# Optimization experiments

Measured on AMD Instinct MI355X. Metric: run time of the kernel, lower is better.

Reference implementation:

```python
import jax, jax.numpy as jnp
import numpy as np

X_SCALE, X_ZP = 0.03, -66.0
Y_SCALE, Y_ZP = 0.025, 160.0  # per-tensor quant params for uint8 y


def setup_inputs() -> dict:
    key = jax.random.key(0)
    kx, ky = jax.random.split(key)
    # x simulates int8 values in [-128, 127], stored as fp32
    x = jax.random.randint(kx, (7, 8, 1024, 1024), 0, 256).astype(jnp.float32) - 128.0
    # y simulates uint8 values in [0, 255], stored as fp32
    y = jax.random.randint(ky, (8, 1024, 1024), 0, 256).astype(jnp.float32)
    return {"x": x, "y": y}


def reference(x, y):
    # dequantize: (q - zero_point) * scale
    qx = (x - X_ZP) * X_SCALE              # [7, B, M, K] fp32
    qy = (y - Y_ZP) * Y_SCALE              # [B, K, N] fp32
    # torch.matmul broadcasting: 4D @ 3D -> [7, B, M, N]
    return jnp.einsum('sbmk,bkn->sbmn', qx, qy)
```

## Files before the change

kernel.cpp:

```cpp
#include <hip/hip_runtime.h>
#include <cstdint>


#define NG 56

typedef int v4i  __attribute__((ext_vector_type(4)));
typedef int v16i __attribute__((ext_vector_type(16)));

#define GLOAD16(g, l) __builtin_amdgcn_global_load_lds( \
    (const __attribute__((address_space(1))) void*)(g), \
    (__attribute__((address_space(3))) void*)(l), 16, 0, 0)

#define MFMA_I8(a, b, c) __builtin_amdgcn_mfma_i32_32x32x32_i8(a, b, c, 0, 0, 0)

typedef __attribute__((address_space(3))) const unsigned char* lds_cptr;

__device__ __forceinline__ v4i lds_read16(lds_cptr p) {
    v4i d;
    asm volatile("ds_read_b128 %0, %1" : "=v"(d) : "v"(p));
    return d;
}

__device__ __forceinline__ unsigned pack4(float4 v, float& s) {
    s += (v.x + v.y) + (v.z + v.w);
    unsigned b0 = __float_as_uint(v.x + 8388736.0f);
    unsigned b1 = __float_as_uint(v.y + 8388736.0f);
    unsigned b2 = __float_as_uint(v.z + 8388736.0f);
    unsigned b3 = __float_as_uint(v.w + 8388736.0f);
    return ((b0 & 0xFFu) | ((b1 & 0xFFu) << 8) | ((b2 & 0xFFu) << 16) | ((b3 & 0xFFu) << 24))
           ^ 0x80808080u;
}

__global__ __launch_bounds__(256) void k_prep_x(const float* __restrict__ x,
                                                unsigned char* __restrict__ xb,
                                                float* __restrict__ rx) {
    int row  = blockIdx.x * 4 + (threadIdx.x >> 6);
    int lane = threadIdx.x & 63;
    const float* src = x + (size_t)row * 1024;
    float s = 0.f;
#pragma unroll
    for (int it = 0; it < 4; ++it) {
        float4 v = *(const float4*)(src + it * 256 + lane * 4);
        unsigned p = pack4(v, s);
        *(unsigned*)&xb[(size_t)row * 1024 + it * 256 + lane * 4] = p;
    }
#pragma unroll
    for (int off = 32; off > 0; off >>= 1) s += __shfl_down(s, off);
    if (lane == 0) rx[row] = s;
}

__global__ __launch_bounds__(256) void k_prep_y(const float* __restrict__ y,
                                                unsigned char* __restrict__ yt,
                                                float* __restrict__ cy) {
    __shared__ float tile[64][65];
    __shared__ float csum[4][64];
    int b  = blockIdx.x >> 8;
    int t  = blockIdx.x & 255;
    int kt = (t >> 4) * 64, nt = (t & 15) * 64;
    int tx = threadIdx.x & 63;
    int ty = threadIdx.x >> 6;
    const float* src = y + ((size_t)b << 20) + (size_t)kt * 1024 + nt;
    float part = 0.f;
#pragma unroll
    for (int r = 0; r < 16; ++r) {
        int kk = r * 4 + ty;
        float v = src[(size_t)kk * 1024 + tx];
        tile[kk][tx] = v;
        part += v;
    }
    csum[ty][tx] = part;
    __syncthreads();
    if (threadIdx.x < 64) {
        float s = csum[0][tx] + csum[1][tx] + csum[2][tx] + csum[3][tx];
        atomicAdd(&cy[b * 1024 + nt + tx], s);
    }
    int ky = threadIdx.x & 15;
    int ny = threadIdx.x >> 4;
#pragma unroll
    for (int r = 0; r < 4; ++r) {
        int nn = r * 16 + ny;
        unsigned b0 = __float_as_uint(tile[ky * 4 + 0][nn] + 8388608.0f);
        unsigned b1 = __float_as_uint(tile[ky * 4 + 1][nn] + 8388608.0f);
        unsigned b2 = __float_as_uint(tile[ky * 4 + 2][nn] + 8388608.0f);
        unsigned b3 = __float_as_uint(tile[ky * 4 + 3][nn] + 8388608.0f);
        unsigned p = ((b0 & 0xFFu) | ((b1 & 0xFFu) << 8) | ((b2 & 0xFFu) << 16) |
                      ((b3 & 0xFFu) << 24)) ^ 0x80808080u;
        *(unsigned*)&yt[((size_t)b << 20) + (size_t)(nt + nn) * 1024 + kt + ky * 4] = p;
    }
}

__global__ __launch_bounds__(512, 2) void k_gemm(const unsigned char* __restrict__ xb,
                                                 const unsigned char* __restrict__ yt,
                                                 const float* __restrict__ rx,
                                                 const float* __restrict__ cy,
                                                 float* __restrict__ out) {
    __shared__ __align__(16) unsigned char As[3][256 * 64];
    __shared__ __align__(16) unsigned char Bs[3][256 * 64];

    int bid = blockIdx.x;
    int wg  = (bid & 7) * 112 + (bid >> 3);
    int g   = wg >> 4;
    int t   = wg & 15;
    int m0  = (t >> 2) * 256, n0 = (t & 3) * 256;
    int b   = g & 7;

    int tid = threadIdx.x, lane = tid & 63, w = tid >> 6;
    int wm = w >> 2, wn = w & 3;

    const unsigned char* Ab = xb + (size_t)g * 1048576 + (size_t)m0 * 1024;
    const unsigned char* Bb = yt + ((size_t)b << 20) + (size_t)n0 * 1024;

    int srow   = tid >> 2;
    int schunk = (tid & 3) ^ ((srow >> 1) & 3);
    size_t offA0 = (size_t)srow * 1024 + (size_t)schunk * 16;
    size_t offA1 = offA0 + 131072;
    int dstA0 = (tid & ~63) * 16;
    int dstA1 = 8192 + (tid & ~63) * 16;

#define GLQ0(rs, kb) GLOAD16(Ab + offA0 + (size_t)(kb), &As[rs][dstA0])
#define GLQ1(rs, kb) GLOAD16(Ab + offA1 + (size_t)(kb), &As[rs][dstA1])
#define GLQ2(rs, kb) GLOAD16(Bb + offA0 + (size_t)(kb), &Bs[rs][dstA0])
#define GLQ3(rs, kb) GLOAD16(Bb + offA1 + (size_t)(kb), &Bs[rs][dstA1])

    v16i acc[4][2];
#pragma unroll
    for (int i = 0; i < 4; ++i)
#pragma unroll
        for (int j = 0; j < 2; ++j)
#pragma unroll
            for (int q = 0; q < 16; ++q) acc[i][j][q] = 0;

    int arow = lane & 31, hi = lane >> 5, key = (lane >> 1) & 3;
    int rA0 = (wm * 128 +  0 + arow) * 64;
    int rA1 = (wm * 128 + 32 + arow) * 64;
    int rA2 = (wm * 128 + 64 + arow) * 64;
    int rA3 = (wm * 128 + 96 + arow) * 64;
    int rB0 = (wn * 64 +  0 + arow) * 64;
    int rB1 = (wn * 64 + 32 + arow) * 64;
    int c0 = (hi ^ key) * 16;
    int c1 = ((2 + hi) ^ key) * 16;

    v4i cA0, cA1, cB0, cB1;
    v4i nA0, nA1, nB0, nB1;

#define VM3 asm volatile("s_waitcnt vmcnt(3)" ::: "memory")
#define VM0 asm volatile("s_waitcnt vmcnt(0)" ::: "memory")
#define NOVM (void)0

#define PHASE(VMS, RN, CK, RAa, RAb, N0, N1, N2, N3, GLS, LGK, HH, C0_, C1_, C2_, C3_) do { \
    VMS;                                                                   \
    __builtin_amdgcn_s_barrier();                                          \
    __builtin_amdgcn_sched_barrier(0);                                     \
    { lds_cptr _ap = (lds_cptr)&As[RN][0];                                 \
      lds_cptr _bp = (lds_cptr)&Bs[RN][0];                                 \
      N0 = lds_read16(_ap + RAa + (CK));                                   \
      N1 = lds_read16(_ap + RAb + (CK));                                   \
      N2 = lds_read16(_bp + rB0 + (CK));                                   \
      N3 = lds_read16(_bp + rB1 + (CK)); }                                 \
    GLS;                                                                   \
    asm volatile("s_waitcnt lgkmcnt(" #LGK ")" ::: "memory");              \
    __builtin_amdgcn_sched_barrier(0);                                     \
    __builtin_amdgcn_s_setprio(1);                                         \
    acc[2*(HH)  ][0] = MFMA_I8(C0_, C2_, acc[2*(HH)  ][0]);                \
    acc[2*(HH)  ][1] = MFMA_I8(C0_, C3_, acc[2*(HH)  ][1]);                \
    acc[2*(HH)+1][0] = MFMA_I8(C1_, C2_, acc[2*(HH)+1][0]);                \
    acc[2*(HH)+1][1] = MFMA_I8(C1_, C3_, acc[2*(HH)+1][1]);                \
    __builtin_amdgcn_s_setprio(0);                                         \
} while (0)

#define TILE(rt, rn, rs, DOST, VMP3) do {                                                       \
    PHASE(NOVM, rt, c0, rA2, rA3, nA0,nA1,nB0,nB1, if (DOST) GLQ0(rs, kb);, 4, 0, cA0,cA1,cB0,cB1); \
    PHASE(NOVM, rt, c1, rA0, rA1, cA0,cA1,cB0,cB1, if (DOST) GLQ1(rs, kb);, 4, 1, nA0,nA1,nB0,nB1); \
    PHASE(NOVM, rt, c1, rA2, rA3, nA0,nA1,nB0,nB1, if (DOST) GLQ2(rs, kb);, 4, 0, cA0,cA1,cB0,cB1); \
    PHASE(VMP3, rn, c0, rA0, rA1, cA0,cA1,cB0,cB1, if (DOST) GLQ3(rs, kb);, 4, 1, nA0,nA1,nB0,nB1); \
} while (0)

    GLQ0(0, 0);  GLQ1(0, 0);  GLQ2(0, 0);  GLQ3(0, 0);
    GLQ0(1, 64); GLQ1(1, 64); GLQ2(1, 64); GLQ3(1, 64);
    VM3; VM0;
    asm volatile("s_waitcnt vmcnt(4)" ::: "memory");
    __builtin_amdgcn_s_barrier();
    __builtin_amdgcn_sched_barrier(0);
    { lds_cptr _ap = (lds_cptr)&As[0][0];
      lds_cptr _bp = (lds_cptr)&Bs[0][0];
      cA0 = lds_read16(_ap + rA0 + c0);
      cA1 = lds_read16(_ap + rA1 + c0);
      cB0 = lds_read16(_bp + rB0 + c0);
      cB1 = lds_read16(_bp + rB1 + c0); }

    int kb = 128;
    for (int u = 0; u < 4; ++u) {
        TILE(0, 1, 2, 1, VM3); kb += 64;
        TILE(1, 2, 0, 1, VM3); kb += 64;
        TILE(2, 0, 1, 1, VM3); kb += 64;
    }
    TILE(0, 1, 2, 1, VM3); kb += 64;
    TILE(1, 2, 0, 1, VM3); kb += 64;
    TILE(2, 0, 1, 0, VM0);
    PHASE(NOVM, 0, c0, rA2, rA3, nA0,nA1,nB0,nB1, NOVM;, 4, 0, cA0,cA1,cB0,cB1);
    PHASE(NOVM, 0, c1, rA0, rA1, cA0,cA1,cB0,cB1, NOVM;, 4, 1, nA0,nA1,nB0,nB1);
    PHASE(NOVM, 0, c1, rA2, rA3, nA0,nA1,nB0,nB1, NOVM;, 4, 0, cA0,cA1,cB0,cB1);
    __builtin_amdgcn_s_barrier();
    __builtin_amdgcn_sched_barrier(0);
    asm volatile("s_waitcnt lgkmcnt(0)" ::: "memory");
    __builtin_amdgcn_sched_barrier(0);
    acc[2][0] = MFMA_I8(nA0, nB0, acc[2][0]);
    acc[2][1] = MFMA_I8(nA0, nB1, acc[2][1]);
    acc[3][0] = MFMA_I8(nA1, nB0, acc[3][0]);
    acc[3][1] = MFMA_I8(nA1, nB1, acc[3][1]);
#undef TILE
#undef PHASE
#undef VM3
#undef VM0
#undef NOVM
#undef GLQ0
#undef GLQ1
#undef GLQ2
#undef GLQ3

    const float* rxp = rx + g * 1024 + m0 + wm * 128;
    const float* cyp = cy + b * 1024 + n0 + wn * 64;
    float* og = out + (size_t)g * 1048576 + (size_t)(m0 + wm * 128) * 1024 + n0 + wn * 64;
    int col = lane & 31, r4 = hi * 4;
#pragma unroll
    for (int fi = 0; fi < 4; ++fi)
#pragma unroll
        for (int fj = 0; fj < 2; ++fj) {
            int cc = fj * 32 + col;
            float cv = cyp[cc];
            v16i v = acc[fi][fj];
#pragma unroll
            for (int q = 0; q < 16; ++q) {
                int rl = (q & 3) + 8 * (q >> 2) + r4;
                float rxv = rxp[fi * 32 + rl];
                og[(size_t)(fi * 32 + rl) * 1024 + cc] =
                    7.5e-4f * ((float)v[q] - 32.0f * rxv + 66.0f * cv - 10813440.0f);
            }
        }
}

__global__ void k_naive(const float* __restrict__ x, const float* __restrict__ y,
                        float* __restrict__ out) {
    int g = blockIdx.z, b = g & 7;
    int tx = threadIdx.x, ty = threadIdx.y;
    int m = blockIdx.y * 16 + ty, n = blockIdx.x * 16 + tx;
    __shared__ float a[16][17], bs[16][17];
    float s = 0.f;
    for (int kt = 0; kt < 64; ++kt) {
        a[ty][tx]  = x[(size_t)g * 1048576 + (size_t)m * 1024 + kt * 16 + tx];
        bs[ty][tx] = y[(size_t)b * 1048576 + (size_t)(kt * 16 + ty) * 1024 + n];
        __syncthreads();
#pragma unroll
        for (int j = 0; j < 16; ++j)
            s += ((a[ty][j] + 66.0f) * 0.03f) * ((bs[j][tx] - 160.0f) * 0.025f);
        __syncthreads();
    }
    out[(size_t)g * 1048576 + (size_t)m * 1024 + n] = s;
}

extern "C" void kernel_launch(void* const* d_in, const int* in_sizes, int n_in,
                              void* d_out, int out_size, void* d_ws, size_t ws_size,
                              hipStream_t stream) {
    const float* x = (const float*)d_in[0];
    const float* y = (const float*)d_in[1];
    float* out = (float*)d_out;

    const size_t CY_OFF = 0;
    const size_t RX_OFF = 32768;
    const size_t YT_OFF = 262144;
    const size_t XB_OFF = 262144 + 8388608ull;
    const size_t NEED   = XB_OFF + 58720256ull;

    if (ws_size >= NEED) {
        float* cy         = (float*)((char*)d_ws + CY_OFF);
        float* rx         = (float*)((char*)d_ws + RX_OFF);
        unsigned char* yt = (unsigned char*)((char*)d_ws + YT_OFF);
        unsigned char* xb = (unsigned char*)((char*)d_ws + XB_OFF);
        hipMemsetAsync(cy, 0, 32768, stream);
        k_prep_x<<<14336, 256, 0, stream>>>(x, xb, rx);
        k_prep_y<<<2048, 256, 0, stream>>>(y, yt, cy);
        k_gemm<<<NG * 16, 512, 0, stream>>>(xb, yt, rx, cy, out);
    } else {
        dim3 grid(64, 64, NG), blk(16, 16);
        k_naive<<<grid, blk, 0, stream>>>(x, y, out);
    }
}
```

Before: 181.9 us.

## Load B fragments directly from global into registers and quad-buffer A in LDS

B is no longer staged through LDS. Each wave now loads its B fragments straight into registers with global_load_dwordx4, double-buffered across K steps, while only A goes through LDS with four stages instead of three. The inner loop is restructured so each step reads all A fragments, issues the next B loads and the A prefetch, then runs 16 MFMAs. This removes the B LDS writes and reads and halves LDS use. In exchange the two waves that share a column of B both fetch it from cache, register pressure rises, and global load latency now sits directly in front of the MFMAs.

Measured after the change: 214.6 us. 1.18x slower.

```diff
diff --git a/kernel.cpp b/kernel.cpp
--- a/kernel.cpp
+++ b/kernel.cpp
@@ -94,8 +94,7 @@
                                                  const float* __restrict__ rx,
                                                  const float* __restrict__ cy,
                                                  float* __restrict__ out) {
-    __shared__ __align__(16) unsigned char As[3][256 * 64];
-    __shared__ __align__(16) unsigned char Bs[3][256 * 64];
+    __shared__ __align__(16) unsigned char As[4][256 * 64];
 
     int bid = blockIdx.x;
     int wg  = (bid & 7) * 112 + (bid >> 3);
@@ -108,7 +107,6 @@
     int wm = w >> 2, wn = w & 3;
 
     const unsigned char* Ab = xb + (size_t)g * 1048576 + (size_t)m0 * 1024;
-    const unsigned char* Bb = yt + ((size_t)b << 20) + (size_t)n0 * 1024;
 
     int srow   = tid >> 2;
     int schunk = (tid & 3) ^ ((srow >> 1) & 3);
@@ -117,10 +115,10 @@
     int dstA0 = (tid & ~63) * 16;
     int dstA1 = 8192 + (tid & ~63) * 16;
 
-#define GLQ0(rs, kb) GLOAD16(Ab + offA0 + (size_t)(kb), &As[rs][dstA0])
-#define GLQ1(rs, kb) GLOAD16(Ab + offA1 + (size_t)(kb), &As[rs][dstA1])
-#define GLQ2(rs, kb) GLOAD16(Bb + offA0 + (size_t)(kb), &Bs[rs][dstA0])
-#define GLQ3(rs, kb) GLOAD16(Bb + offA1 + (size_t)(kb), &Bs[rs][dstA1])
+#define STAGE(buf, kbyte) do {                                    \
+    GLOAD16(Ab + offA0 + (size_t)(kbyte), &As[buf][dstA0]);       \
+    GLOAD16(Ab + offA1 + (size_t)(kbyte), &As[buf][dstA1]);       \
+} while (0)
 
     v16i acc[4][2];
 #pragma unroll
@@ -135,88 +133,80 @@
     int rA1 = (wm * 128 + 32 + arow) * 64;
     int rA2 = (wm * 128 + 64 + arow) * 64;
     int rA3 = (wm * 128 + 96 + arow) * 64;
-    int rB0 = (wn * 64 +  0 + arow) * 64;
-    int rB1 = (wn * 64 + 32 + arow) * 64;
     int c0 = (hi ^ key) * 16;
     int c1 = ((2 + hi) ^ key) * 16;
 
-    v4i cA0, cA1, cB0, cB1;
-    v4i nA0, nA1, nB0, nB1;
-
-#define VM3 asm volatile("s_waitcnt vmcnt(3)" ::: "memory")
-#define VM0 asm volatile("s_waitcnt vmcnt(0)" ::: "memory")
-#define NOVM (void)0
-
-#define PHASE(VMS, RN, CK, RAa, RAb, N0, N1, N2, N3, GLS, LGK, HH, C0_, C1_, C2_, C3_) do { \
-    VMS;                                                                   \
-    __builtin_amdgcn_s_barrier();                                          \
-    __builtin_amdgcn_sched_barrier(0);                                     \
-    { lds_cptr _ap = (lds_cptr)&As[RN][0];                                 \
-      lds_cptr _bp = (lds_cptr)&Bs[RN][0];                                 \
-      N0 = lds_read16(_ap + RAa + (CK));                                   \
-      N1 = lds_read16(_ap + RAb + (CK));                                   \
-      N2 = lds_read16(_bp + rB0 + (CK));                                   \
-      N3 = lds_read16(_bp + rB1 + (CK)); }                                 \
-    GLS;                                                                   \
-    asm volatile("s_waitcnt lgkmcnt(" #LGK ")" ::: "memory");              \
-    __builtin_amdgcn_sched_barrier(0);                                     \
-    __builtin_amdgcn_s_setprio(1);                                         \
-    acc[2*(HH)  ][0] = MFMA_I8(C0_, C2_, acc[2*(HH)  ][0]);                \
-    acc[2*(HH)  ][1] = MFMA_I8(C0_, C3_, acc[2*(HH)  ][1]);                \
-    acc[2*(HH)+1][0] = MFMA_I8(C1_, C2_, acc[2*(HH)+1][0]);                \
-    acc[2*(HH)+1][1] = MFMA_I8(C1_, C3_, acc[2*(HH)+1][1]);                \
-    __builtin_amdgcn_s_setprio(0);                                         \
+    const unsigned char* Bbl = yt + ((size_t)b << 20)
+                             + (size_t)(n0 + wn * 64 + arow) * 1024 + hi * 16;
+
+#define LOADB(R0, R1, R2, R3, kbyte) do {                                             \
+    const unsigned char* _bp = Bbl + (size_t)(kbyte);                                 \
+    asm volatile("global_load_dwordx4 %0, %1, off" : "=&v"(R0) : "v"(_bp) : "memory");          \
+    asm volatile("global_load_dwordx4 %0, %1, off" : "=&v"(R1) : "v"(_bp + 32) : "memory");     \
+    asm volatile("global_load_dwordx4 %0, %1, off" : "=&v"(R2) : "v"(_bp + 32768) : "memory");  \
+    asm volatile("global_load_dwordx4 %0, %1, off" : "=&v"(R3) : "v"(_bp + 32800) : "memory");  \
 } while (0)
 
-#define TILE(rt, rn, rs, DOST, VMP3) do {                                                       \
-    PHASE(NOVM, rt, c0, rA2, rA3, nA0,nA1,nB0,nB1, if (DOST) GLQ0(rs, kb);, 4, 0, cA0,cA1,cB0,cB1); \
-    PHASE(NOVM, rt, c1, rA0, rA1, cA0,cA1,cB0,cB1, if (DOST) GLQ1(rs, kb);, 4, 1, nA0,nA1,nB0,nB1); \
-    PHASE(NOVM, rt, c1, rA2, rA3, nA0,nA1,nB0,nB1, if (DOST) GLQ2(rs, kb);, 4, 0, cA0,cA1,cB0,cB1); \
-    PHASE(VMP3, rn, c0, rA0, rA1, cA0,cA1,cB0,cB1, if (DOST) GLQ3(rs, kb);, 4, 1, nA0,nA1,nB0,nB1); \
+#define STEP(T, VMN, BU0, BU1, BU2, BU3, BL0, BL1, BL2, BL3, DOLB, DOST) do { \
+    asm volatile("s_waitcnt vmcnt(" #VMN ")" ::: "memory");                   \
+    __builtin_amdgcn_s_barrier();                                             \
+    __builtin_amdgcn_sched_barrier(0);                                        \
+    lds_cptr _ap = (lds_cptr)&As[(T) & 3][0];                                 \
+    v4i a00 = lds_read16(_ap + rA0 + c0);                                     \
+    v4i a10 = lds_read16(_ap + rA1 + c0);                                     \
+    v4i a20 = lds_read16(_ap + rA2 + c0);                                     \
+    v4i a30 = lds_read16(_ap + rA3 + c0);                                     \
+    v4i a01 = lds_read16(_ap + rA0 + c1);                                     \
+    v4i a11 = lds_read16(_ap + rA1 + c1);                                     \
+    v4i a21 = lds_read16(_ap + rA2 + c1);                                     \
+    v4i a31 = lds_read16(_ap + rA3 + c1);                                     \
+    if (DOLB) { LOADB(BL0, BL1, BL2, BL3, ((T) + 1) * 64); }                  \
+    __builtin_amdgcn_sched_barrier(0);                                        \
+    if (DOST) { STAGE(((T) + 3) & 3, ((T) + 3) * 64); }                       \
+    __builtin_amdgcn_sched_barrier(0);                                        \
+    asm volatile("s_waitcnt lgkmcnt(0)" ::: "memory");                        \
+    __builtin_amdgcn_sched_barrier(0);                                        \
+    __builtin_amdgcn_s_setprio(1);                                            \
+    acc[0][0] = MFMA_I8(a00, BU0, acc[0][0]);                                 \
+    acc[1][0] = MFMA_I8(a10, BU0, acc[1][0]);                                 \
+    acc[2][0] = MFMA_I8(a20, BU0, acc[2][0]);                                 \
+    acc[3][0] = MFMA_I8(a30, BU0, acc[3][0]);                                 \
+    acc[0][1] = MFMA_I8(a00, BU2, acc[0][1]);                                 \
+    acc[1][1] = MFMA_I8(a10, BU2, acc[1][1]);                                 \
+    acc[2][1] = MFMA_I8(a20, BU2, acc[2][1]);                                 \
+    acc[3][1] = MFMA_I8(a30, BU2, acc[3][1]);                                 \
+    acc[0][0] = MFMA_I8(a01, BU1, acc[0][0]);                                 \
+    acc[1][0] = MFMA_I8(a11, BU1, acc[1][0]);                                 \
+    acc[2][0] = MFMA_I8(a21, BU1, acc[2][0]);                                 \
+    acc[3][0] = MFMA_I8(a31, BU1, acc[3][0]);                                 \
+    acc[0][1] = MFMA_I8(a01, BU3, acc[0][1]);                                 \
+    acc[1][1] = MFMA_I8(a11, BU3, acc[1][1]);                                 \
+    acc[2][1] = MFMA_I8(a21, BU3, acc[2][1]);                                 \
+    acc[3][1] = MFMA_I8(a31, BU3, acc[3][1]);                                 \
+    __builtin_amdgcn_s_setprio(0);                                            \
 } while (0)
 
-    GLQ0(0, 0);  GLQ1(0, 0);  GLQ2(0, 0);  GLQ3(0, 0);
-    GLQ0(1, 64); GLQ1(1, 64); GLQ2(1, 64); GLQ3(1, 64);
-    VM3; VM0;
-    asm volatile("s_waitcnt vmcnt(4)" ::: "memory");
-    __builtin_amdgcn_s_barrier();
+    v4i bA0, bA1, bA2, bA3;
+    v4i bB0, bB1, bB2, bB3;
+
+    STAGE(0, 0);
+    STAGE(1, 64);
     __builtin_amdgcn_sched_barrier(0);
-    { lds_cptr _ap = (lds_cptr)&As[0][0];
-      lds_cptr _bp = (lds_cptr)&Bs[0][0];
-      cA0 = lds_read16(_ap + rA0 + c0);
-      cA1 = lds_read16(_ap + rA1 + c0);
-      cB0 = lds_read16(_bp + rB0 + c0);
-      cB1 = lds_read16(_bp + rB1 + c0); }
-
-    int kb = 128;
-    for (int u = 0; u < 4; ++u) {
-        TILE(0, 1, 2, 1, VM3); kb += 64;
-        TILE(1, 2, 0, 1, VM3); kb += 64;
-        TILE(2, 0, 1, 1, VM3); kb += 64;
-    }
-    TILE(0, 1, 2, 1, VM3); kb += 64;
-    TILE(1, 2, 0, 1, VM3); kb += 64;
-    TILE(2, 0, 1, 0, VM0);
-    PHASE(NOVM, 0, c0, rA2, rA3, nA0,nA1,nB0,nB1, NOVM;, 4, 0, cA0,cA1,cB0,cB1);
-    PHASE(NOVM, 0, c1, rA0, rA1, cA0,cA1,cB0,cB1, NOVM;, 4, 1, nA0,nA1,nB0,nB1);
-    PHASE(NOVM, 0, c1, rA2, rA3, nA0,nA1,nB0,nB1, NOVM;, 4, 0, cA0,cA1,cB0,cB1);
-    __builtin_amdgcn_s_barrier();
+    LOADB(bA0, bA1, bA2, bA3, 0);
     __builtin_amdgcn_sched_barrier(0);
-    asm volatile("s_waitcnt lgkmcnt(0)" ::: "memory");
+    STAGE(2, 128);
     __builtin_amdgcn_sched_barrier(0);
-    acc[2][0] = MFMA_I8(nA0, nB0, acc[2][0]);
-    acc[2][1] = MFMA_I8(nA0, nB1, acc[2][1]);
-    acc[3][0] = MFMA_I8(nA1, nB0, acc[3][0]);
-    acc[3][1] = MFMA_I8(nA1, nB1, acc[3][1]);
-#undef TILE
-#undef PHASE
-#undef VM3
-#undef VM0
-#undef NOVM
-#undef GLQ0
-#undef GLQ1
-#undef GLQ2
-#undef GLQ3
+
+#pragma unroll 1
+    for (int T = 0; T < 14; T += 2) {
+        STEP(T,     2, bA0, bA1, bA2, bA3, bB0, bB1, bB2, bB3, 1, (T < 13));
+        STEP(T + 1, 2, bB0, bB1, bB2, bB3, bA0, bA1, bA2, bA3, 1, (T + 1 < 13));
+    }
+    STEP(14, 0, bA0, bA1, bA2, bA3, bB0, bB1, bB2, bB3, 1, 0);
+    STEP(15, 0, bB0, bB1, bB2, bB3, bA0, bA1, bA2, bA3, 0, 0);
+#undef STEP
+#undef LOADB
+#undef STAGE
 
     const float* rxp = rx + g * 1024 + m0 + wm * 128;
     const float* cyp = cy + b * 1024 + n0 + wn * 64;
```
